# Kernel tuning notes

Measured on AMD Instinct MI355X. Metric: run time of the kernel, lower is better.

## Reference

```python
import jax, jax.numpy as jnp
import numpy as np

MEM_SIZE = 2048
CELL = 64
R_HEADS = 4
IN_SIZE = 512
IFACE = CELL * R_HEADS + CELL + 2 * CELL + 2 * R_HEADS + 5  # 461
DELTA = 1e-6
EPS = 1e-6


def setup_inputs() -> dict:
    key = jax.random.key(0)
    ks = jax.random.split(key, 8)
    b = 256
    return {
        'xi': jax.random.normal(ks[0], (b, IN_SIZE), jnp.float32),
        'W': jax.random.normal(ks[1], (IFACE, IN_SIZE), jnp.float32) * 0.05,
        'gamma': jnp.ones((IFACE,), jnp.float32),
        'beta': jnp.zeros((IFACE,), jnp.float32),
        'memory': jax.random.normal(ks[2], (b, MEM_SIZE, CELL), jnp.float32),
        'read_weights': jax.random.uniform(ks[3], (b, R_HEADS, MEM_SIZE), jnp.float32),
        'write_weights': jax.random.uniform(ks[4], (b, 1, MEM_SIZE), jnp.float32),
        'usage': jax.random.uniform(ks[5], (b, MEM_SIZE), jnp.float32),
    }


def _cosine(mem, keys):
    # mem: (b,m,c), keys: (b,k,c) -> (b,k,m)
    mem_n = mem / (jnp.linalg.norm(mem, axis=-1, keepdims=True) + EPS)
    key_n = keys / (jnp.linalg.norm(keys, axis=-1, keepdims=True) + EPS)
    return jnp.einsum('bkc,bmc->bkm', key_n, mem_n)


def reference(xi, W, gamma, beta, memory, read_weights, write_weights, usage):
    b = xi.shape[0]
    r, k, w, m = R_HEADS, CELL, CELL, MEM_SIZE

    # interface projection + GroupNorm(1, C) over channel dim
    itf = xi @ W.T
    mu = jnp.mean(itf, axis=1, keepdims=True)
    var = jnp.var(itf, axis=1, keepdims=True)
    itf = (itf - mu) / jnp.sqrt(var + 1e-5) * gamma + beta

    c = 0
    read_keys = jnp.tanh(itf[:, c:c + r * k].reshape(b, r, k)); c += r * k
    read_strengths = jax.nn.softplus(itf[:, c:c + r]); c += r
    write_key = jnp.tanh(itf[:, c:c + k].reshape(b, 1, k)); c += k
    write_strength = jax.nn.softplus(itf[:, c]).reshape(b, 1); c += 1
    erase_vec = jax.nn.sigmoid(itf[:, c:c + w].reshape(b, 1, w)); c += w
    write_vec = jnp.tanh(itf[:, c:c + w].reshape(b, 1, w)); c += w
    free_gates = jax.nn.sigmoid(itf[:, c:c + r]); c += r
    alloc_gate = jax.nn.softmax(itf[:, c:c + 3], axis=1); c += 3
    write_gate = jax.nn.sigmoid(itf[:, c]).reshape(b, 1)

    # ---- usage update ----
    u = usage + (1 - usage) * (1 - jnp.prod(1 - write_weights, axis=1))
    psi = jnp.prod(1 - free_gates[:, :, None] * read_weights, axis=1)  # (b,m)
    u = u * psi

    # ---- content weighting for write ----
    wcw = jax.nn.softmax(_cosine(memory, write_key) * write_strength[:, :, None], axis=2)  # (b,1,m)

    # ---- allocation ----
    u2 = DELTA + (1 - DELTA) * u
    idx = jnp.argsort(u2, axis=1)                              # ascending usage (phi)
    su = jnp.take_along_axis(u2, idx, axis=1)                  # sorted usage
    cp = jnp.cumprod(jnp.concatenate([jnp.ones((b, 1), u2.dtype), su], axis=1), axis=1)[:, :-1]
    sa = (1 - su) * cp
    inv = jnp.argsort(idx, axis=1)                             # inverse permutation (phi_rev)
    alloc = jnp.take_along_axis(sa, inv, axis=1)               # (b,m)

    # ---- write weighting ----
    fw = (alloc_gate[:, 0:1] * jnp.mean(read_weights, axis=1)
          + alloc_gate[:, 1:2] * alloc
          + alloc_gate[:, 2:3] * wcw[:, 0])
    ww = (write_gate * fw)[:, None, :]                         # (b,1,m)

    # ---- memory write (erase + add) ----
    reset_gate = jnp.prod(1 - ww[:, :, :, None] * erase_vec[:, :, None, :], axis=1)  # (b,m,w)
    mem = memory * reset_gate + jnp.einsum('bm,bw->bmw', ww[:, 0], write_vec[:, 0])

    # ---- read ----
    rw = jax.nn.softmax(_cosine(mem, read_keys) * read_strengths[:, :, None], axis=2)  # (b,r,m)
    read_vectors = jnp.einsum('brm,bmw->brw', rw, mem)         # (b,r,w)
    return read_vectors
```

## Files before the change

### kernel.cpp

```cpp
#include <hip/hip_runtime.h>
#include <math.h>

#define MM    2048
#define CC    64
#define RH    4
#define NIF   461
#define INS   512
#define EPSN  1e-6f

typedef unsigned long long u64;

#define OFF_P     ((size_t)0)
#define OFF_U2    ((size_t)131072)
#define OFF_MRW   ((size_t)655360)
#define OFF_ALLOC ((size_t)1179648)
#define OFF_SCAL  ((size_t)1703936)

__global__ __launch_bounds__(512) void k1_interface(
    const float* __restrict__ xi, const float* __restrict__ W,
    const float* __restrict__ gamma, const float* __restrict__ beta,
    const float* __restrict__ read_w, const float* __restrict__ write_w,
    const float* __restrict__ usage, float* __restrict__ ws)
{
  const int b = blockIdx.x, tid = threadIdx.x;
  const int lane = tid & 63, wid = tid >> 6;
  __shared__ __align__(16) float s_xi[512], s_itf[512], s_act[512];
  __shared__ float sRed[24];

  s_xi[tid] = xi[(size_t)b*INS + tid];
  __syncthreads();

  {
    const float4 x0 = ((const float4*)s_xi)[lane*2];
    const float4 x1 = ((const float4*)s_xi)[lane*2+1];
    for (int col = wid; col < NIF; col += 8) {
      const float4* Wr = (const float4*)(W + (size_t)col*INS);
      float4 a0 = Wr[lane*2], a1 = Wr[lane*2+1];
      float p = a0.x*x0.x + a0.y*x0.y + a0.z*x0.z + a0.w*x0.w
              + a1.x*x1.x + a1.y*x1.y + a1.z*x1.z + a1.w*x1.w;
      #pragma unroll
      for (int off=1; off<64; off<<=1) p += __shfl_xor(p, off);
      if (lane==0) s_itf[col] = p;
    }
  }
  __syncthreads();

  {
    float v = (tid < NIF) ? s_itf[tid] : 0.f;
    float s = v, q = v*v;
    #pragma unroll
    for (int off=1; off<64; off<<=1) { s += __shfl_xor(s,off); q += __shfl_xor(q,off); }
    if (lane==0){ sRed[wid] = s; sRed[8+wid] = q; }
    __syncthreads();
    if (tid==0){
      float ts=0.f, tq=0.f;
      for (int i=0;i<8;i++){ ts+=sRed[i]; tq+=sRed[8+i]; }
      float mean = ts/(float)NIF;
      float var  = tq/(float)NIF - mean*mean;
      sRed[16]=mean; sRed[17]=rsqrtf(var+1e-5f);
    }
    __syncthreads();
    float mean = sRed[16], rstd = sRed[17];
    if (tid < NIF) {
      float g = (s_itf[tid]-mean)*rstd*gamma[tid] + beta[tid];
      float a;
      if      (tid < 256) a = tanhf(g);
      else if (tid < 260) a = fmaxf(g,0.f) + log1pf(expf(-fabsf(g)));
      else if (tid < 324) a = tanhf(g);
      else if (tid ==324) a = fmaxf(g,0.f) + log1pf(expf(-fabsf(g)));
      else if (tid < 389) a = 1.f/(1.f+expf(-g));
      else if (tid < 453) a = tanhf(g);
      else if (tid < 457) a = 1.f/(1.f+expf(-g));
      else if (tid < 460) a = g;
      else                a = 1.f/(1.f+expf(-g));
      s_act[tid] = a;
    }
  }
  __syncthreads();

  float* P = ws + OFF_P + (size_t)b*512;
  if (wid < 4) {
    float t = s_act[wid*64 + lane];
    float q = t*t;
    #pragma unroll
    for (int off=1; off<64; off<<=1) q += __shfl_xor(q,off);
    P[wid*64+lane] = t * (s_act[256+wid] / (sqrtf(q) + EPSN));
  } else if (wid == 4) {
    float t = s_act[260+lane];
    float q = t*t;
    #pragma unroll
    for (int off=1; off<64; off<<=1) q += __shfl_xor(q,off);
    P[256+lane] = t * (s_act[324] / (sqrtf(q) + EPSN));
  } else if (wid == 5) {
    P[320+lane] = s_act[325+lane];
    P[384+lane] = s_act[389+lane];
  } else if (wid == 6 && lane == 0) {
    float a0=s_act[457], a1=s_act[458], a2=s_act[459];
    float mx = fmaxf(a0, fmaxf(a1,a2));
    float e0=expf(a0-mx), e1=expf(a1-mx), e2=expf(a2-mx);
    float is = 1.f/(e0+e1+e2);
    P[448]=e0*is; P[449]=e1*is; P[450]=e2*is; P[451]=s_act[460];
  }

  {
    const float4* us4 = (const float4*)(usage   + (size_t)b*MM);
    const float4* wr4 = (const float4*)(write_w + (size_t)b*MM);
    const float4* rw4 = (const float4*)(read_w  + (size_t)b*RH*MM);
    const float fg0=s_act[453], fg1=s_act[454], fg2=s_act[455], fg3=s_act[456];
    float4 u = us4[tid], w = wr4[tid];
    float4 r0 = rw4[tid], r1 = rw4[512+tid], r2 = rw4[1024+tid], r3 = rw4[1536+tid];
    float4 mr, u2o;
    mr.x = 0.25f*(r0.x+r1.x+r2.x+r3.x);
    mr.y = 0.25f*(r0.y+r1.y+r2.y+r3.y);
    mr.z = 0.25f*(r0.z+r1.z+r2.z+r3.z);
    mr.w = 0.25f*(r0.w+r1.w+r2.w+r3.w);
    #define U2C(comp)                                                           \
    { float uu  = u.comp + (1.f-u.comp)*w.comp;                                 \
      float psi = (1.f-fg0*r0.comp)*(1.f-fg1*r1.comp)*(1.f-fg2*r2.comp)*(1.f-fg3*r3.comp); \
      u2o.comp = 1e-6f + (1.f-1e-6f)*(uu*psi); }
    U2C(x) U2C(y) U2C(z) U2C(w)
    #undef U2C
    ((float4*)(ws + OFF_MRW + (size_t)b*MM))[tid] = mr;
    ((float4*)(ws + OFF_U2  + (size_t)b*MM))[tid] = u2o;
  }
}

__global__ __launch_bounds__(256) void k2_fused(
    const float* __restrict__ memory, float* __restrict__ ws)
{
  __shared__ __align__(16) u64 sKeys[2048];
  __shared__ float sT[260];
  const int tid = threadIdx.x;

  if (blockIdx.x < 256) {
    const int b = blockIdx.x;
    const int lane = tid & 63, w = tid >> 6;
    const float* u2p = ws + OFF_U2 + (size_t)b*MM;
    for (int i = tid; i < MM; i += 256)
      sKeys[i] = ((u64)__float_as_uint(u2p[i])<<32) | (unsigned)i;
    __syncthreads();

    for (int k = 2; k <= MM; k <<= 1) {
      for (int j = k >> 1; j > 0; j >>= 1) {
        #pragma unroll 4
        for (int c = tid; c < MM/2; c += 256) {
          int i   = ((c & ~(j-1)) << 1) | (c & (j-1));
          int ixj = i | j;
          u64 a = sKeys[i], d = sKeys[ixj];
          bool up = ((i & k) == 0);
          if ((a > d) == up) { sKeys[i] = d; sKeys[ixj] = a; }
        }
        __syncthreads();
      }
    }

    float p[8];
    {
      float run = 1.f;
      #pragma unroll
      for (int e = 0; e < 8; ++e) {
        float su = __uint_as_float((unsigned)(sKeys[tid*8+e]>>32));
        run *= su; p[e] = run;
      }
      sT[tid] = run;
    }
    __syncthreads();
    float v = sT[tid];
    float incl = v;
    #pragma unroll
    for (int off=1; off<64; off<<=1) {
      float n = __shfl_up(incl, off);
      if (lane >= off) incl *= n;
    }
    float excl = __shfl_up(incl, 1);
    if (lane == 0) excl = 1.f;
    if (lane == 63) sT[256 + w] = incl;
    __syncthreads();
    float base = 1.f;
    for (int ww2 = 0; ww2 < w; ++ww2) base *= sT[256 + ww2];
    float E = base * excl;

    float* allocp = ws + OFF_ALLOC + (size_t)b*MM;
    #pragma unroll
    for (int e = 0; e < 8; ++e) {
      u64 kk = sKeys[tid*8+e];
      float su = __uint_as_float((unsigned)(kk>>32));
      unsigned idx = (unsigned)(kk & 0xFFFFFFFFu);
      float cp = E * (e ? p[e-1] : 1.f);
      allocp[idx] = (1.f - su) * cp;
    }
  } else {
    const int f = blockIdx.x - 256;
    const int b = f >> 3, slice = f & 7;
    const int q = tid & 7, rowg = tid >> 3;
    const float* P = ws + OFF_P + (size_t)b*512;
    const float4 wkA = ((const float4*)(P+256))[q*2], wkB = ((const float4*)(P+256))[q*2+1];
    const float4 eA  = ((const float4*)(P+320))[q*2], eB  = ((const float4*)(P+320))[q*2+1];
    const float4 wvA = ((const float4*)(P+384))[q*2], wvB = ((const float4*)(P+384))[q*2+1];
    const float4 k0A = ((const float4*)P)[      q*2], k0B = ((const float4*)P)[      q*2+1];
    const float4 k1A = ((const float4*)P)[ 16 + q*2], k1B = ((const float4*)P)[ 16 + q*2+1];
    const float4 k2A = ((const float4*)P)[ 32 + q*2], k2B = ((const float4*)P)[ 32 + q*2+1];
    const float4 k3A = ((const float4*)P)[ 48 + q*2], k3B = ((const float4*)P)[ 48 + q*2+1];
    const float4* mem4 = (const float4*)(memory + (size_t)b*MM*CC) + (size_t)slice*256*16;
    float4* sc4 = (float4*)(ws + OFF_SCAL) + ((size_t)b*MM + slice*256)*4;

    for (int it = 0; it < 8; ++it) {
      int m = it*32 + rowg;
      float4 vA = mem4[m*16 + q*2], vB = mem4[m*16 + q*2+1];
      float4 veA, veB;
      veA.x=vA.x*eA.x; veA.y=vA.y*eA.y; veA.z=vA.z*eA.z; veA.w=vA.w*eA.w;
      veB.x=vB.x*eB.x; veB.y=vB.y*eB.y; veB.z=vB.z*eB.z; veB.w=vB.w*eB.w;
      #define DOT(a,b) (a.x*b.x + a.y*b.y + a.z*b.z + a.w*b.w)
      float S  = DOT(vA,wkA) + DOT(vB,wkB);
      float A  = DOT(vA,vA)  + DOT(vB,vB);
      float B  = DOT(veA,vA) + DOT(veB,vB);
      float C  = DOT(veA,veA)+ DOT(veB,veB);
      float D  = DOT(vA,wvA) + DOT(vB,wvB);
      float E  = DOT(veA,wvA)+ DOT(veB,wvB);
      float G0 = DOT(vA,k0A) + DOT(vB,k0B);
      float G1 = DOT(vA,k1A) + DOT(vB,k1B);
      float G2 = DOT(vA,k2A) + DOT(vB,k2B);
      float G3 = DOT(vA,k3A) + DOT(vB,k3B);
      float H0 = DOT(veA,k0A)+ DOT(veB,k0B);
      float H1 = DOT(veA,k1A)+ DOT(veB,k1B);
      float H2 = DOT(veA,k2A)+ DOT(veB,k2B);
      float H3 = DOT(veA,k3A)+ DOT(veB,k3B);
      #undef DOT
      #pragma unroll
      for (int off=1; off<8; off<<=1) {
        S += __shfl_xor(S,off);   A += __shfl_xor(A,off);
        B += __shfl_xor(B,off);   C += __shfl_xor(C,off);
        D += __shfl_xor(D,off);   E += __shfl_xor(E,off);
        G0 += __shfl_xor(G0,off); G1 += __shfl_xor(G1,off);
        G2 += __shfl_xor(G2,off); G3 += __shfl_xor(G3,off);
        H0 += __shfl_xor(H0,off); H1 += __shfl_xor(H1,off);
        H2 += __shfl_xor(H2,off); H3 += __shfl_xor(H3,off);
      }
      if (q == 0) {
        float4 o0; o0.x=S;  o0.y=A;  o0.z=B;  o0.w=C;
        float4 o1; o1.x=D;  o1.y=E;  o1.z=0;  o1.w=0;
        float4 o2; o2.x=G0; o2.y=G1; o2.z=G2; o2.w=G3;
        float4 o3; o3.x=H0; o3.y=H1; o3.z=H2; o3.w=H3;
        sc4[m*4+0]=o0; sc4[m*4+1]=o1; sc4[m*4+2]=o2; sc4[m*4+3]=o3;
      }
    }
  }
}

__global__ __launch_bounds__(256) void k3_fused(
    const float* __restrict__ memory, float* __restrict__ ws,
    float* __restrict__ out)
{
  const int slice = blockIdx.x >> 8, b = blockIdx.x & 255;
  const int tid = threadIdx.x, lane = tid & 63, w = tid >> 6;
  __shared__ __align__(16) float bufA[2048];
  __shared__ float bufB[256*5];
  __shared__ __align__(16) float ldsP[4*16*32];
  __shared__ float sR[48];
  __shared__ float sKF[8];

  const float* P = ws + OFF_P + (size_t)b*512;
  const float4* sc4 = (const float4*)(ws + OFF_SCAL + (size_t)b*MM*16);

  if (tid < 64) {
    float wv = P[384+tid];
    float p0=wv*P[tid], p1=wv*P[64+tid], p2=wv*P[128+tid], p3=wv*P[192+tid], f=wv*wv;
    #pragma unroll
    for (int off=1; off<64; off<<=1) {
      p0+=__shfl_xor(p0,off); p1+=__shfl_xor(p1,off); p2+=__shfl_xor(p2,off);
      p3+=__shfl_xor(p3,off); f+=__shfl_xor(f,off);
    }
    if (tid==0){ sKF[0]=p0; sKF[1]=p1; sKF[2]=p2; sKF[3]=p3; sKF[4]=f; }
  }

  float ls = 0.f;
  #pragma unroll
  for (int k = 0; k < 8; ++k) {
    int m = tid + k*256;
    float4 s0 = sc4[m*4];
    float ew = expf(s0.x / (sqrtf(s0.y)+EPSN));
    bufA[m] = ew;
    ls += ew;
  }
  #pragma unroll
  for (int off=1; off<64; off<<=1) ls += __shfl_xor(ls,off);
  if (lane==0) sR[w] = ls;
  __syncthreads();
  const float invW = 1.f/(sR[0]+sR[1]+sR[2]+sR[3]);

  const float ag0=P[448], ag1=P[449], ag2=P[450], wg=P[451];
  const float K0=sKF[0], K1=sKF[1], K2=sKF[2], K3=sKF[3], F=sKF[4];
  const float* mrwp = ws + OFF_MRW   + (size_t)b*MM;
  const float* alp  = ws + OFF_ALLOC + (size_t)b*MM;

  float h0=0.f,h1=0.f,h2=0.f,h3=0.f, g0=0.f,g1=0.f,g2=0.f,g3=0.f;
  #pragma unroll
  for (int k = 0; k < 8; ++k) {
    int m = tid + k*256;
    float wwv = wg*(ag0*mrwp[m] + ag1*alp[m] + ag2*bufA[m]*invW);
    float4 s0 = sc4[m*4], s1 = sc4[m*4+1], sG = sc4[m*4+2], sH = sc4[m*4+3];
    float nsq = s0.y + 2.f*wwv*(s1.x - s0.z) + wwv*wwv*(s0.w - 2.f*s1.y + F);
    float rstd = 1.f/(sqrtf(fmaxf(nsq,0.f))+EPSN);
    float e0 = expf((sG.x + wwv*(K0 - sH.x))*rstd);
    float e1 = expf((sG.y + wwv*(K1 - sH.y))*rstd);
    float e2 = expf((sG.z + wwv*(K2 - sH.z))*rstd);
    float e3 = expf((sG.w + wwv*(K3 - sH.w))*rstd);
    h0+=e0; h1+=e1; h2+=e2; h3+=e3;
    g0+=e0*wwv; g1+=e1*wwv; g2+=e2*wwv; g3+=e3*wwv;
    if (k == slice) {
      bufB[tid]=e0; bufB[256+tid]=e1; bufB[512+tid]=e2; bufB[768+tid]=e3;
      bufB[1024+tid]=wwv;
    }
  }
  #pragma unroll
  for (int off=1; off<64; off<<=1) {
    h0+=__shfl_xor(h0,off); h1+=__shfl_xor(h1,off);
    h2+=__shfl_xor(h2,off); h3+=__shfl_xor(h3,off);
    g0+=__shfl_xor(g0,off); g1+=__shfl_xor(g1,off);
    g2+=__shfl_xor(g2,off); g3+=__shfl_xor(g3,off);
  }
  if (lane==0){
    sR[8 +w*8+0]=h0; sR[8 +w*8+1]=h1; sR[8 +w*8+2]=h2; sR[8 +w*8+3]=h3;
    sR[8 +w*8+4]=g0; sR[8 +w*8+5]=g1; sR[8 +w*8+6]=g2; sR[8 +w*8+7]=g3;
  }
  __syncthreads();
  const float i0 = 1.f/(sR[8] +sR[16]+sR[24]+sR[32]);
  const float i1 = 1.f/(sR[9] +sR[17]+sR[25]+sR[33]);
  const float i2 = 1.f/(sR[10]+sR[18]+sR[26]+sR[34]);
  const float i3 = 1.f/(sR[11]+sR[19]+sR[27]+sR[35]);
  const float cr0 = (sR[12]+sR[20]+sR[28]+sR[36])*i0;
  const float cr1 = (sR[13]+sR[21]+sR[29]+sR[37])*i1;
  const float cr2 = (sR[14]+sR[22]+sR[30]+sR[38])*i2;
  const float cr3 = (sR[15]+sR[23]+sR[31]+sR[39])*i3;

  {
    float e0=bufB[tid], e1=bufB[256+tid], e2=bufB[512+tid], e3=bufB[768+tid];
    float wwv=bufB[1024+tid];
    float a0=e0*i0, a1=e1*i1, a2=e2*i2, a3=e3*i3;
    bufA[tid*8+0]=a0; bufA[tid*8+1]=a1; bufA[tid*8+2]=a2; bufA[tid*8+3]=a3;
    bufA[tid*8+4]=a0*wwv; bufA[tid*8+5]=a1*wwv; bufA[tid*8+6]=a2*wwv; bufA[tid*8+7]=a3*wwv;
  }
  __syncthreads();

  const int rq = lane >> 4, cq = lane & 15;
  const float4* mem4 = (const float4*)(memory + (size_t)b*MM*CC) + (size_t)slice*256*16;
  float4 acc[8];
  #pragma unroll
  for (int j=0;j<8;++j){ acc[j].x=0;acc[j].y=0;acc[j].z=0;acc[j].w=0; }
  #pragma unroll 4
  for (int i = 0; i < 16; ++i) {
    int m = w*64 + i*4 + rq;
    float4 v = mem4[m*16 + cq];
    float4 wa = *(const float4*)&bufA[m*8];
    float4 wb = *(const float4*)&bufA[m*8+4];
    #define ACC(j, s) { acc[j].x += (s)*v.x; acc[j].y += (s)*v.y; acc[j].z += (s)*v.z; acc[j].w += (s)*v.w; }
    ACC(0, wa.x) ACC(1, wa.y) ACC(2, wa.z) ACC(3, wa.w)
    ACC(4, wb.x) ACC(5, wb.y) ACC(6, wb.z) ACC(7, wb.w)
    #undef ACC
  }
  #pragma unroll
  for (int j=0;j<8;++j){
    #pragma unroll
    for (int off=16; off<64; off<<=1) {
      acc[j].x += __shfl_xor(acc[j].x, off);
      acc[j].y += __shfl_xor(acc[j].y, off);
      acc[j].z += __shfl_xor(acc[j].z, off);
      acc[j].w += __shfl_xor(acc[j].w, off);
    }
  }
  if (rq == 0) {
    float4* p4 = (float4*)&ldsP[(w*16 + cq)*32];
    #pragma unroll
    for (int j=0;j<8;++j) p4[j] = acc[j];
  }
  __syncthreads();

  {
    int jj = tid >> 6;
    int c  = tid & 63;
    int cq2 = c >> 2, ci = c & 3;
    float s1 = 0.f, s2 = 0.f;
    #pragma unroll
    for (int g=0; g<4; ++g) {
      s1 += ldsP[(g*16 + cq2)*32 +  jj*4    + ci];
      s2 += ldsP[(g*16 + cq2)*32 + (jj+4)*4 + ci];
    }
    float crv = (jj==0)?cr0:((jj==1)?cr1:((jj==2)?cr2:cr3));
    float val = s1 - P[320+c]*s2 + crv*P[384+c]*0.125f;
    atomicAdd(&out[((size_t)b<<8) + jj*64 + c], val);
  }
}

extern "C" void kernel_launch(void* const* d_in, const int* in_sizes, int n_in,
                              void* d_out, int out_size, void* d_ws, size_t ws_size,
                              hipStream_t stream) {
  const float* xi      = (const float*)d_in[0];
  const float* W       = (const float*)d_in[1];
  const float* gamma   = (const float*)d_in[2];
  const float* beta    = (const float*)d_in[3];
  const float* memory  = (const float*)d_in[4];
  const float* read_w  = (const float*)d_in[5];
  const float* write_w = (const float*)d_in[6];
  const float* usage   = (const float*)d_in[7];
  float* ws  = (float*)d_ws;
  float* out = (float*)d_out;

  hipMemsetAsync(out, 0, (size_t)out_size*sizeof(float), stream);
  k1_interface<<<dim3(256), dim3(512), 0, stream>>>(xi, W, gamma, beta, read_w, write_w, usage, ws);
  k2_fused   <<<dim3(2304), dim3(256), 0, stream>>>(memory, ws);
  k3_fused   <<<dim3(2048), dim3(256), 0, stream>>>(memory, ws, out);
}
```

Before: 155.9 us.

## Fuse all stages into one cooperative persistent kernel with grid syncs

```diff
diff --git a/kernel.cpp b/kernel.cpp
--- a/kernel.cpp
+++ b/kernel.cpp
@@ -1,9 +1,11 @@
 #include <hip/hip_runtime.h>
+#include <hip/hip_cooperative_groups.h>
 #include <math.h>
+
+namespace cg = cooperative_groups;
 
 #define MM    2048
 #define CC    64
-#define RH    4
 #define NIF   461
 #define INS   512
 #define EPSN  1e-6f
@@ -11,162 +13,176 @@
 typedef unsigned long long u64;
 
 #define OFF_P     ((size_t)0)
-#define OFF_U2    ((size_t)131072)
-#define OFF_MRW   ((size_t)655360)
-#define OFF_ALLOC ((size_t)1179648)
-#define OFF_SCAL  ((size_t)1703936)
-
-__global__ __launch_bounds__(512) void k1_interface(
+#define OFF_ITF   ((size_t)131072)
+#define OFF_ALLOC ((size_t)249856)
+#define OFF_MRW   ((size_t)774144)
+#define OFF_SUMS  ((size_t)1298432)
+#define OFF_SCAL  ((size_t)1302528)
+#define OFF_W8    ((size_t)9691136)
+
+__device__ __forceinline__ float actfn(int c, float g){
+  if (c < 256)  return tanhf(g);
+  if (c < 260)  return fmaxf(g,0.f) + log1pf(expf(-fabsf(g)));
+  if (c < 324)  return tanhf(g);
+  if (c == 324) return fmaxf(g,0.f) + log1pf(expf(-fabsf(g)));
+  if (c < 389)  return 1.f/(1.f+expf(-g));
+  if (c < 453)  return tanhf(g);
+  if (c < 457)  return 1.f/(1.f+expf(-g));
+  if (c < 460)  return g;
+  return 1.f/(1.f+expf(-g));
+}
+
+__global__ __launch_bounds__(256,2) void dnc_all(
     const float* __restrict__ xi, const float* __restrict__ W,
     const float* __restrict__ gamma, const float* __restrict__ beta,
-    const float* __restrict__ read_w, const float* __restrict__ write_w,
-    const float* __restrict__ usage, float* __restrict__ ws)
+    const float* __restrict__ memory, const float* __restrict__ read_w,
+    const float* __restrict__ write_w, const float* __restrict__ usage,
+    float* __restrict__ ws, float* __restrict__ out)
 {
-  const int b = blockIdx.x, tid = threadIdx.x;
-  const int lane = tid & 63, wid = tid >> 6;
-  __shared__ __align__(16) float s_xi[512], s_itf[512], s_act[512];
-  __shared__ float sRed[24];
-
-  s_xi[tid] = xi[(size_t)b*INS + tid];
+  cg::grid_group grid = cg::this_grid();
+  const int bid = blockIdx.x, tid = threadIdx.x;
+  const int lane = tid & 63, wvid = tid >> 6;
+  const int b = bid & 255, half = bid >> 8;
+
+  __shared__ __align__(16) unsigned char sMem[19456];
+  __shared__ float sR[64];
+  u64*   keysL = (u64*)sMem;
+  float* sTL   = (float*)(sMem + 16384);
+  float* sactL = (float*)(sMem + 17424);
+  float* sxiL  = (float*)sMem;
+  float* sW8   = (float*)sMem;
+  float* ldsP  = (float*)(sMem + 8192);
+
+  if (tid < 128) out[((size_t)bid<<7) + tid] = 0.f;
+  if (bid < 256 && tid < 16) ws[OFF_SUMS + (size_t)bid*16 + tid] = 0.f;
+  sxiL[tid]     = xi[(size_t)b*INS + tid];
+  sxiL[tid+256] = xi[(size_t)b*INS + tid + 256];
   __syncthreads();
-
   {
-    const float4 x0 = ((const float4*)s_xi)[lane*2];
-    const float4 x1 = ((const float4*)s_xi)[lane*2+1];
-    for (int col = wid; col < NIF; col += 8) {
+    const float4 x0 = ((const float4*)sxiL)[lane*2];
+    const float4 x1 = ((const float4*)sxiL)[lane*2+1];
+    const int cbase = half*232;
+    const int cend  = (cbase+232 < NIF) ? cbase+232 : NIF;
+    for (int col = cbase + wvid; col < cend; col += 4) {
       const float4* Wr = (const float4*)(W + (size_t)col*INS);
       float4 a0 = Wr[lane*2], a1 = Wr[lane*2+1];
       float p = a0.x*x0.x + a0.y*x0.y + a0.z*x0.z + a0.w*x0.w
               + a1.x*x1.x + a1.y*x1.y + a1.z*x1.z + a1.w*x1.w;
       #pragma unroll
       for (int off=1; off<64; off<<=1) p += __shfl_xor(p, off);
-      if (lane==0) s_itf[col] = p;
+      if (lane==0) ws[OFF_ITF + (size_t)b*464 + col] = p;
     }
   }
-  __syncthreads();
-
-  {
-    float v = (tid < NIF) ? s_itf[tid] : 0.f;
-    float s = v, q = v*v;
+  __threadfence();
+  grid.sync();
+
+  if (bid < 256) {
+    const float* itf = ws + OFF_ITF + (size_t)b*464;
+    float v1 = (tid < NIF) ? itf[tid] : 0.f;
+    float v2 = (tid+256 < NIF) ? itf[tid+256] : 0.f;
+    float s = v1+v2, q = v1*v1+v2*v2;
     #pragma unroll
-    for (int off=1; off<64; off<<=1) { s += __shfl_xor(s,off); q += __shfl_xor(q,off); }
-    if (lane==0){ sRed[wid] = s; sRed[8+wid] = q; }
+    for (int off=1; off<64; off<<=1){ s += __shfl_xor(s,off); q += __shfl_xor(q,off); }
+    if (lane==0){ sR[wvid]=s; sR[8+wvid]=q; }
     __syncthreads();
     if (tid==0){
-      float ts=0.f, tq=0.f;
-      for (int i=0;i<8;i++){ ts+=sRed[i]; tq+=sRed[8+i]; }
+      float ts=sR[0]+sR[1]+sR[2]+sR[3], tq=sR[8]+sR[9]+sR[10]+sR[11];
       float mean = ts/(float)NIF;
       float var  = tq/(float)NIF - mean*mean;
-      sRed[16]=mean; sRed[17]=rsqrtf(var+1e-5f);
-    }
-    __syncthreads();
-    float mean = sRed[16], rstd = sRed[17];
-    if (tid < NIF) {
-      float g = (s_itf[tid]-mean)*rstd*gamma[tid] + beta[tid];
-      float a;
-      if      (tid < 256) a = tanhf(g);
-      else if (tid < 260) a = fmaxf(g,0.f) + log1pf(expf(-fabsf(g)));
-      else if (tid < 324) a = tanhf(g);
-      else if (tid ==324) a = fmaxf(g,0.f) + log1pf(expf(-fabsf(g)));
-      else if (tid < 389) a = 1.f/(1.f+expf(-g));
-      else if (tid < 453) a = tanhf(g);
-      else if (tid < 457) a = 1.f/(1.f+expf(-g));
-      else if (tid < 460) a = g;
-      else                a = 1.f/(1.f+expf(-g));
-      s_act[tid] = a;
-    }
-  }
-  __syncthreads();
-
-  float* P = ws + OFF_P + (size_t)b*512;
-  if (wid < 4) {
-    float t = s_act[wid*64 + lane];
-    float q = t*t;
-    #pragma unroll
-    for (int off=1; off<64; off<<=1) q += __shfl_xor(q,off);
-    P[wid*64+lane] = t * (s_act[256+wid] / (sqrtf(q) + EPSN));
-  } else if (wid == 4) {
-    float t = s_act[260+lane];
-    float q = t*t;
-    #pragma unroll
-    for (int off=1; off<64; off<<=1) q += __shfl_xor(q,off);
-    P[256+lane] = t * (s_act[324] / (sqrtf(q) + EPSN));
-  } else if (wid == 5) {
-    P[320+lane] = s_act[325+lane];
-    P[384+lane] = s_act[389+lane];
-  } else if (wid == 6 && lane == 0) {
-    float a0=s_act[457], a1=s_act[458], a2=s_act[459];
-    float mx = fmaxf(a0, fmaxf(a1,a2));
-    float e0=expf(a0-mx), e1=expf(a1-mx), e2=expf(a2-mx);
-    float is = 1.f/(e0+e1+e2);
-    P[448]=e0*is; P[449]=e1*is; P[450]=e2*is; P[451]=s_act[460];
-  }
-
-  {
-    const float4* us4 = (const float4*)(usage   + (size_t)b*MM);
-    const float4* wr4 = (const float4*)(write_w + (size_t)b*MM);
-    const float4* rw4 = (const float4*)(read_w  + (size_t)b*RH*MM);
-    const float fg0=s_act[453], fg1=s_act[454], fg2=s_act[455], fg3=s_act[456];
-    float4 u = us4[tid], w = wr4[tid];
-    float4 r0 = rw4[tid], r1 = rw4[512+tid], r2 = rw4[1024+tid], r3 = rw4[1536+tid];
-    float4 mr, u2o;
-    mr.x = 0.25f*(r0.x+r1.x+r2.x+r3.x);
-    mr.y = 0.25f*(r0.y+r1.y+r2.y+r3.y);
-    mr.z = 0.25f*(r0.z+r1.z+r2.z+r3.z);
-    mr.w = 0.25f*(r0.w+r1.w+r2.w+r3.w);
-    #define U2C(comp)                                                           \
-    { float uu  = u.comp + (1.f-u.comp)*w.comp;                                 \
-      float psi = (1.f-fg0*r0.comp)*(1.f-fg1*r1.comp)*(1.f-fg2*r2.comp)*(1.f-fg3*r3.comp); \
-      u2o.comp = 1e-6f + (1.f-1e-6f)*(uu*psi); }
-    U2C(x) U2C(y) U2C(z) U2C(w)
-    #undef U2C
-    ((float4*)(ws + OFF_MRW + (size_t)b*MM))[tid] = mr;
-    ((float4*)(ws + OFF_U2  + (size_t)b*MM))[tid] = u2o;
-  }
-}
-
-__global__ __launch_bounds__(256) void k2_fused(
-    const float* __restrict__ memory, float* __restrict__ ws)
-{
-  __shared__ __align__(16) u64 sKeys[2048];
-  __shared__ float sT[260];
-  const int tid = threadIdx.x;
-
-  if (blockIdx.x < 256) {
-    const int b = blockIdx.x;
-    const int lane = tid & 63, w = tid >> 6;
-    const float* u2p = ws + OFF_U2 + (size_t)b*MM;
-    for (int i = tid; i < MM; i += 256)
-      sKeys[i] = ((u64)__float_as_uint(u2p[i])<<32) | (unsigned)i;
-    __syncthreads();
-
-    for (int k = 2; k <= MM; k <<= 1) {
-      for (int j = k >> 1; j > 0; j >>= 1) {
+      sR[16]=mean; sR[17]=rsqrtf(var+1e-5f);
+    }
+    __syncthreads();
+    float mean=sR[16], rstd=sR[17];
+    if (tid < NIF)     sactL[tid]     = actfn(tid,     (v1-mean)*rstd*gamma[tid]    +beta[tid]);
+    if (tid+256 < NIF) sactL[tid+256] = actfn(tid+256, (v2-mean)*rstd*gamma[tid+256]+beta[tid+256]);
+    __syncthreads();
+
+    float* P = ws + OFF_P + (size_t)b*512;
+    {
+      float t0 = sactL[wvid*64 + lane];
+      float qq = t0*t0;
+      #pragma unroll
+      for (int off=1; off<64; off<<=1) qq += __shfl_xor(qq,off);
+      float fk = t0 * (sactL[256+wvid]/(sqrtf(qq)+EPSN));
+      P[wvid*64+lane] = fk;
+      float kk = fk * sactL[389+lane];
+      #pragma unroll
+      for (int off=1; off<64; off<<=1) kk += __shfl_xor(kk,off);
+      if (lane==0) P[452+wvid] = kk;
+    }
+    if (wvid==0) {
+      float t0 = sactL[260+lane];
+      float qq = t0*t0;
+      #pragma unroll
+      for (int off=1; off<64; off<<=1) qq += __shfl_xor(qq,off);
+      P[256+lane] = t0 * (sactL[324]/(sqrtf(qq)+EPSN));
+      float wvv = sactL[389+lane];
+      float ff = wvv*wvv;
+      #pragma unroll
+      for (int off=1; off<64; off<<=1) ff += __shfl_xor(ff,off);
+      if (lane==0) P[456]=ff;
+    } else if (wvid==1) {
+      P[320+lane] = sactL[325+lane];
+    } else if (wvid==2) {
+      P[384+lane] = sactL[389+lane];
+    } else if (wvid==3 && lane==0) {
+      float a0=sactL[457], a1=sactL[458], a2=sactL[459];
+      float mx = fmaxf(a0, fmaxf(a1,a2));
+      float e0=expf(a0-mx), e1=expf(a1-mx), e2=expf(a2-mx);
+      float is = 1.f/(e0+e1+e2);
+      P[448]=e0*is; P[449]=e1*is; P[450]=e2*is; P[451]=sactL[460];
+    }
+    {
+      const float4* us4 = (const float4*)(usage   + (size_t)b*MM);
+      const float4* wr4 = (const float4*)(write_w + (size_t)b*MM);
+      const float4* rw4 = (const float4*)(read_w  + (size_t)b*4*MM);
+      const float fg0=sactL[453], fg1=sactL[454], fg2=sactL[455], fg3=sactL[456];
+      #pragma unroll
+      for (int k=0;k<2;k++){
+        int i4 = tid + k*256;
+        float4 u = us4[i4], w2 = wr4[i4];
+        float4 r0 = rw4[i4], r1 = rw4[512+i4], r2 = rw4[1024+i4], r3 = rw4[1536+i4];
+        float4 mr;
+        mr.x = 0.25f*(r0.x+r1.x+r2.x+r3.x);
+        mr.y = 0.25f*(r0.y+r1.y+r2.y+r3.y);
+        mr.z = 0.25f*(r0.z+r1.z+r2.z+r3.z);
+        mr.w = 0.25f*(r0.w+r1.w+r2.w+r3.w);
+        ((float4*)(ws + OFF_MRW + (size_t)b*MM))[i4] = mr;
+        #define U2C(comp, off)                                                   \
+        { float uu  = u.comp + (1.f-u.comp)*w2.comp;                             \
+          float psi = (1.f-fg0*r0.comp)*(1.f-fg1*r1.comp)*(1.f-fg2*r2.comp)*(1.f-fg3*r3.comp); \
+          float u2v = 1e-6f + (1.f-1e-6f)*(uu*psi);                              \
+          keysL[i4*4+off] = ((u64)__float_as_uint(u2v)<<32) | (unsigned)(i4*4+off); }
+        U2C(x,0) U2C(y,1) U2C(z,2) U2C(w,3)
+        #undef U2C
+      }
+    }
+    __syncthreads();
+    for (int k2 = 2; k2 <= MM; k2 <<= 1) {
+      for (int j = k2 >> 1; j > 0; j >>= 1) {
         #pragma unroll 4
         for (int c = tid; c < MM/2; c += 256) {
           int i   = ((c & ~(j-1)) << 1) | (c & (j-1));
           int ixj = i | j;
-          u64 a = sKeys[i], d = sKeys[ixj];
-          bool up = ((i & k) == 0);
-          if ((a > d) == up) { sKeys[i] = d; sKeys[ixj] = a; }
+          u64 a = keysL[i], d = keysL[ixj];
+          bool up = ((i & k2) == 0);
+          if ((a > d) == up) { keysL[i] = d; keysL[ixj] = a; }
         }
         __syncthreads();
       }
     }
-
-    float p[8];
+    float p8[8];
     {
       float run = 1.f;
       #pragma unroll
-      for (int e = 0; e < 8; ++e) {
-        float su = __uint_as_float((unsigned)(sKeys[tid*8+e]>>32));
-        run *= su; p[e] = run;
-      }
-      sT[tid] = run;
-    }
-    __syncthreads();
-    float v = sT[tid];
-    float incl = v;
+      for (int e=0;e<8;++e){
+        float su = __uint_as_float((unsigned)(keysL[tid*8+e]>>32));
+        run *= su; p8[e] = run;
+      }
+      sTL[tid] = run;
+    }
+    __syncthreads();
+    float vv = sTL[tid], incl = vv;
     #pragma unroll
     for (int off=1; off<64; off<<=1) {
       float n = __shfl_up(incl, off);
@@ -174,26 +190,27 @@
     }
     float excl = __shfl_up(incl, 1);
     if (lane == 0) excl = 1.f;
-    if (lane == 63) sT[256 + w] = incl;
+    if (lane == 63) sTL[256 + wvid] = incl;
     __syncthreads();
     float base = 1.f;
-    for (int ww2 = 0; ww2 < w; ++ww2) base *= sT[256 + ww2];
-    float E = base * excl;
-
+    for (int w2i = 0; w2i < wvid; ++w2i) base *= sTL[256 + w2i];
+    float Ex = base * excl;
     float* allocp = ws + OFF_ALLOC + (size_t)b*MM;
     #pragma unroll
-    for (int e = 0; e < 8; ++e) {
-      u64 kk = sKeys[tid*8+e];
+    for (int e=0;e<8;++e){
+      u64 kk = keysL[tid*8+e];
       float su = __uint_as_float((unsigned)(kk>>32));
       unsigned idx = (unsigned)(kk & 0xFFFFFFFFu);
-      float cp = E * (e ? p[e-1] : 1.f);
+      float cp = Ex * (e ? p8[e-1] : 1.f);
       allocp[idx] = (1.f - su) * cp;
     }
-  } else {
-    const int f = blockIdx.x - 256;
-    const int b = f >> 3, slice = f & 7;
+  }
+  __threadfence();
+  grid.sync();
+
+  {
+    const float* P = ws + OFF_P + (size_t)b*512;
     const int q = tid & 7, rowg = tid >> 3;
-    const float* P = ws + OFF_P + (size_t)b*512;
     const float4 wkA = ((const float4*)(P+256))[q*2], wkB = ((const float4*)(P+256))[q*2+1];
     const float4 eA  = ((const float4*)(P+320))[q*2], eB  = ((const float4*)(P+320))[q*2+1];
     const float4 wvA = ((const float4*)(P+384))[q*2], wvB = ((const float4*)(P+384))[q*2+1];
@@ -201,193 +218,177 @@
     const float4 k1A = ((const float4*)P)[ 16 + q*2], k1B = ((const float4*)P)[ 16 + q*2+1];
     const float4 k2A = ((const float4*)P)[ 32 + q*2], k2B = ((const float4*)P)[ 32 + q*2+1];
     const float4 k3A = ((const float4*)P)[ 48 + q*2], k3B = ((const float4*)P)[ 48 + q*2+1];
-    const float4* mem4 = (const float4*)(memory + (size_t)b*MM*CC) + (size_t)slice*256*16;
-    float4* sc4 = (float4*)(ws + OFF_SCAL) + ((size_t)b*MM + slice*256)*4;
-
-    for (int it = 0; it < 8; ++it) {
-      int m = it*32 + rowg;
-      float4 vA = mem4[m*16 + q*2], vB = mem4[m*16 + q*2+1];
-      float4 veA, veB;
-      veA.x=vA.x*eA.x; veA.y=vA.y*eA.y; veA.z=vA.z*eA.z; veA.w=vA.w*eA.w;
-      veB.x=vB.x*eB.x; veB.y=vB.y*eB.y; veB.z=vB.z*eB.z; veB.w=vB.w*eB.w;
-      #define DOT(a,b) (a.x*b.x + a.y*b.y + a.z*b.z + a.w*b.w)
-      float S  = DOT(vA,wkA) + DOT(vB,wkB);
-      float A  = DOT(vA,vA)  + DOT(vB,vB);
-      float B  = DOT(veA,vA) + DOT(veB,vB);
-      float C  = DOT(veA,veA)+ DOT(veB,veB);
-      float D  = DOT(vA,wvA) + DOT(vB,wvB);
-      float E  = DOT(veA,wvA)+ DOT(veB,wvB);
-      float G0 = DOT(vA,k0A) + DOT(vB,k0B);
-      float G1 = DOT(vA,k1A) + DOT(vB,k1B);
-      float G2 = DOT(vA,k2A) + DOT(vB,k2B);
-      float G3 = DOT(vA,k3A) + DOT(vB,k3B);
-      float H0 = DOT(veA,k0A)+ DOT(veB,k0B);
-      float H1 = DOT(veA,k1A)+ DOT(veB,k1B);
-      float H2 = DOT(veA,k2A)+ DOT(veB,k2B);
-      float H3 = DOT(veA,k3A)+ DOT(veB,k3B);
-      #undef DOT
-      #pragma unroll
-      for (int off=1; off<8; off<<=1) {
-        S += __shfl_xor(S,off);   A += __shfl_xor(A,off);
-        B += __shfl_xor(B,off);   C += __shfl_xor(C,off);
-        D += __shfl_xor(D,off);   E += __shfl_xor(E,off);
-        G0 += __shfl_xor(G0,off); G1 += __shfl_xor(G1,off);
-        G2 += __shfl_xor(G2,off); G3 += __shfl_xor(G3,off);
-        H0 += __shfl_xor(H0,off); H1 += __shfl_xor(H1,off);
-        H2 += __shfl_xor(H2,off); H3 += __shfl_xor(H3,off);
-      }
-      if (q == 0) {
-        float4 o0; o0.x=S;  o0.y=A;  o0.z=B;  o0.w=C;
-        float4 o1; o1.x=D;  o1.y=E;  o1.z=0;  o1.w=0;
-        float4 o2; o2.x=G0; o2.y=G1; o2.z=G2; o2.w=G3;
-        float4 o3; o3.x=H0; o3.y=H1; o3.z=H2; o3.w=H3;
-        sc4[m*4+0]=o0; sc4[m*4+1]=o1; sc4[m*4+2]=o2; sc4[m*4+3]=o3;
-      }
-    }
+    const float4* mem4 = (const float4*)(memory + (size_t)b*MM*CC);
+    float4* scal4 = (float4*)(ws + OFF_SCAL) + (size_t)b*2048*4;
+    float ewsum = 0.f;
+    for (int si=0; si<4; ++si) {
+      const int s = half*4 + si;
+      for (int it=0; it<8; ++it) {
+        int m = it*32 + rowg;
+        int mg = s*256 + m;
+        float4 vA = mem4[mg*16 + q*2], vB = mem4[mg*16 + q*2+1];
+        float4 veA, veB;
+        veA.x=vA.x*eA.x; veA.y=vA.y*eA.y; veA.z=vA.z*eA.z; veA.w=vA.w*eA.w;
+        veB.x=vB.x*eB.x; veB.y=vB.y*eB.y; veB.z=vB.z*eB.z; veB.w=vB.w*eB.w;
+        #define DOT(a,c) (a.x*c.x + a.y*c.y + a.z*c.z + a.w*c.w)
+        float S  = DOT(vA,wkA) + DOT(vB,wkB);
+        float A  = DOT(vA,vA)  + DOT(vB,vB);
+        float B  = DOT(veA,vA) + DOT(veB,vB);
+        float C  = DOT(veA,veA)+ DOT(veB,veB);
+        float D  = DOT(vA,wvA) + DOT(vB,wvB);
+        float E  = DOT(veA,wvA)+ DOT(veB,wvB);
+        float G0 = DOT(vA,k0A) + DOT(vB,k0B);
+        float G1 = DOT(vA,k1A) + DOT(vB,k1B);
+        float G2 = DOT(vA,k2A) + DOT(vB,k2B);
+        float G3 = DOT(vA,k3A) + DOT(vB,k3B);
+        float H0 = DOT(veA,k0A)+ DOT(veB,k0B);
+        float H1 = DOT(veA,k1A)+ DOT(veB,k1B);
+        float H2 = DOT(veA,k2A)+ DOT(veB,k2B);
+        float H3 = DOT(veA,k3A)+ DOT(veB,k3B);
+        #undef DOT
+        #pragma unroll
+        for (int off=1; off<8; off<<=1) {
+          S += __shfl_xor(S,off);   A += __shfl_xor(A,off);
+          B += __shfl_xor(B,off);   C += __shfl_xor(C,off);
+          D += __shfl_xor(D,off);   E += __shfl_xor(E,off);
+          G0 += __shfl_xor(G0,off); G1 += __shfl_xor(G1,off);
+          G2 += __shfl_xor(G2,off); G3 += __shfl_xor(G3,off);
+          H0 += __shfl_xor(H0,off); H1 += __shfl_xor(H1,off);
+          H2 += __shfl_xor(H2,off); H3 += __shfl_xor(H3,off);
+        }
+        if (q == 0) {
+          float ew = expf(S / (sqrtf(A)+EPSN));
+          ewsum += ew;
+          float4 o0; o0.x=S;  o0.y=A;  o0.z=B;  o0.w=C;
+          float4 o1; o1.x=D;  o1.y=E;  o1.z=ew; o1.w=0.f;
+          float4 o2; o2.x=G0; o2.y=G1; o2.z=G2; o2.w=G3;
+          float4 o3; o3.x=H0; o3.y=H1; o3.z=H2; o3.w=H3;
+          scal4[mg*4+0]=o0; scal4[mg*4+1]=o1; scal4[mg*4+2]=o2; scal4[mg*4+3]=o3;
+        }
+      }
+    }
+    #pragma unroll
+    for (int off=1; off<64; off<<=1) ewsum += __shfl_xor(ewsum,off);
+    __syncthreads();
+    if (lane==0) sR[wvid] = ewsum;
+    __syncthreads();
+    if (tid==0) atomicAdd(&ws[OFF_SUMS + (size_t)b*16], sR[0]+sR[1]+sR[2]+sR[3]);
   }
-}
-
-__global__ __launch_bounds__(256) void k3_fused(
-    const float* __restrict__ memory, float* __restrict__ ws,
-    float* __restrict__ out)
-{
-  const int slice = blockIdx.x >> 8, b = blockIdx.x & 255;
-  const int tid = threadIdx.x, lane = tid & 63, w = tid >> 6;
-  __shared__ __align__(16) float bufA[2048];
-  __shared__ float bufB[256*5];
-  __shared__ __align__(16) float ldsP[4*16*32];
-  __shared__ float sR[48];
-  __shared__ float sKF[8];
-
-  const float* P = ws + OFF_P + (size_t)b*512;
-  const float4* sc4 = (const float4*)(ws + OFF_SCAL + (size_t)b*MM*16);
-
-  if (tid < 64) {
-    float wv = P[384+tid];
-    float p0=wv*P[tid], p1=wv*P[64+tid], p2=wv*P[128+tid], p3=wv*P[192+tid], f=wv*wv;
+  __threadfence();
+  grid.sync();
+
+  {
+    const float* P = ws + OFF_P + (size_t)b*512;
+    const float ag0=P[448], ag1=P[449], ag2=P[450], wg=P[451];
+    const float K0=P[452], K1=P[453], K2v=P[454], K3v=P[455], F=P[456];
+    const float invW = 1.f / ws[OFF_SUMS + (size_t)b*16];
+    float h[4]={0,0,0,0}, g[4]={0,0,0,0};
+    for (int si=0; si<4; ++si) {
+      const int r = (half*4+si)*256 + tid;
+      const float4* row = (const float4*)(ws + OFF_SCAL) + ((size_t)b*2048 + r)*4;
+      float4 s0=row[0], s1=row[1], sG=row[2], sH=row[3];
+      float al = ws[OFF_ALLOC + (size_t)b*MM + r];
+      float mr = ws[OFF_MRW   + (size_t)b*MM + r];
+      float wwv = wg*(ag0*mr + ag1*al + ag2*s1.z*invW);
+      float nsq = s0.y + 2.f*wwv*(s1.x - s0.z) + wwv*wwv*(s0.w - 2.f*s1.y + F);
+      float rstd = 1.f/(sqrtf(fmaxf(nsq,0.f))+EPSN);
+      float e0 = expf((sG.x + wwv*(K0 -sH.x))*rstd);
+      float e1 = expf((sG.y + wwv*(K1 -sH.y))*rstd);
+      float e2 = expf((sG.z + wwv*(K2v-sH.z))*rstd);
+      float e3 = expf((sG.w + wwv*(K3v-sH.w))*rstd);
+      float4 oa; oa.x=e0; oa.y=e1; oa.z=e2; oa.w=e3;
+      float4 og; og.x=e0*wwv; og.y=e1*wwv; og.z=e2*wwv; og.w=e3*wwv;
+      float4* w84 = (float4*)(ws + OFF_W8) + ((size_t)b*2048 + r)*2;
+      w84[0]=oa; w84[1]=og;
+      h[0]+=e0; h[1]+=e1; h[2]+=e2; h[3]+=e3;
+      g[0]+=og.x; g[1]+=og.y; g[2]+=og.z; g[3]+=og.w;
+    }
     #pragma unroll
     for (int off=1; off<64; off<<=1) {
-      p0+=__shfl_xor(p0,off); p1+=__shfl_xor(p1,off); p2+=__shfl_xor(p2,off);
-      p3+=__shfl_xor(p3,off); f+=__shfl_xor(f,off);
-    }
-    if (tid==0){ sKF[0]=p0; sKF[1]=p1; sKF[2]=p2; sKF[3]=p3; sKF[4]=f; }
+      #pragma unroll
+      for (int r2=0;r2<4;++r2){ h[r2]+=__shfl_xor(h[r2],off); g[r2]+=__shfl_xor(g[r2],off); }
+    }
+    __syncthreads();
+    if (lane==0){
+      #pragma unroll
+      for (int r2=0;r2<4;++r2){ sR[wvid*8+r2]=h[r2]; sR[wvid*8+4+r2]=g[r2]; }
+    }
+    __syncthreads();
+    if (tid < 8){
+      float ssum = sR[tid] + sR[8+tid] + sR[16+tid] + sR[24+tid];
+      atomicAdd(&ws[OFF_SUMS + (size_t)b*16 + 1 + tid], ssum);
+    }
   }
-
-  float ls = 0.f;
-  #pragma unroll
-  for (int k = 0; k < 8; ++k) {
-    int m = tid + k*256;
-    float4 s0 = sc4[m*4];
-    float ew = expf(s0.x / (sqrtf(s0.y)+EPSN));
-    bufA[m] = ew;
-    ls += ew;
-  }
-  #pragma unroll
-  for (int off=1; off<64; off<<=1) ls += __shfl_xor(ls,off);
-  if (lane==0) sR[w] = ls;
-  __syncthreads();
-  const float invW = 1.f/(sR[0]+sR[1]+sR[2]+sR[3]);
-
-  const float ag0=P[448], ag1=P[449], ag2=P[450], wg=P[451];
-  const float K0=sKF[0], K1=sKF[1], K2=sKF[2], K3=sKF[3], F=sKF[4];
-  const float* mrwp = ws + OFF_MRW   + (size_t)b*MM;
-  const float* alp  = ws + OFF_ALLOC + (size_t)b*MM;
-
-  float h0=0.f,h1=0.f,h2=0.f,h3=0.f, g0=0.f,g1=0.f,g2=0.f,g3=0.f;
-  #pragma unroll
-  for (int k = 0; k < 8; ++k) {
-    int m = tid + k*256;
-    float wwv = wg*(ag0*mrwp[m] + ag1*alp[m] + ag2*bufA[m]*invW);
-    float4 s0 = sc4[m*4], s1 = sc4[m*4+1], sG = sc4[m*4+2], sH = sc4[m*4+3];
-    float nsq = s0.y + 2.f*wwv*(s1.x - s0.z) + wwv*wwv*(s0.w - 2.f*s1.y + F);
-    float rstd = 1.f/(sqrtf(fmaxf(nsq,0.f))+EPSN);
-    float e0 = expf((sG.x + wwv*(K0 - sH.x))*rstd);
-    float e1 = expf((sG.y + wwv*(K1 - sH.y))*rstd);
-    float e2 = expf((sG.z + wwv*(K2 - sH.z))*rstd);
-    float e3 = expf((sG.w + wwv*(K3 - sH.w))*rstd);
-    h0+=e0; h1+=e1; h2+=e2; h3+=e3;
-    g0+=e0*wwv; g1+=e1*wwv; g2+=e2*wwv; g3+=e3*wwv;
-    if (k == slice) {
-      bufB[tid]=e0; bufB[256+tid]=e1; bufB[512+tid]=e2; bufB[768+tid]=e3;
-      bufB[1024+tid]=wwv;
-    }
-  }
-  #pragma unroll
-  for (int off=1; off<64; off<<=1) {
-    h0+=__shfl_xor(h0,off); h1+=__shfl_xor(h1,off);
-    h2+=__shfl_xor(h2,off); h3+=__shfl_xor(h3,off);
-    g0+=__shfl_xor(g0,off); g1+=__shfl_xor(g1,off);
-    g2+=__shfl_xor(g2,off); g3+=__shfl_xor(g3,off);
-  }
-  if (lane==0){
-    sR[8 +w*8+0]=h0; sR[8 +w*8+1]=h1; sR[8 +w*8+2]=h2; sR[8 +w*8+3]=h3;
-    sR[8 +w*8+4]=g0; sR[8 +w*8+5]=g1; sR[8 +w*8+6]=g2; sR[8 +w*8+7]=g3;
-  }
-  __syncthreads();
-  const float i0 = 1.f/(sR[8] +sR[16]+sR[24]+sR[32]);
-  const float i1 = 1.f/(sR[9] +sR[17]+sR[25]+sR[33]);
-  const float i2 = 1.f/(sR[10]+sR[18]+sR[26]+sR[34]);
-  const float i3 = 1.f/(sR[11]+sR[19]+sR[27]+sR[35]);
-  const float cr0 = (sR[12]+sR[20]+sR[28]+sR[36])*i0;
-  const float cr1 = (sR[13]+sR[21]+sR[29]+sR[37])*i1;
-  const float cr2 = (sR[14]+sR[22]+sR[30]+sR[38])*i2;
-  const float cr3 = (sR[15]+sR[23]+sR[31]+sR[39])*i3;
+  __threadfence();
+  grid.sync();
 
   {
-    float e0=bufB[tid], e1=bufB[256+tid], e2=bufB[512+tid], e3=bufB[768+tid];
-    float wwv=bufB[1024+tid];
-    float a0=e0*i0, a1=e1*i1, a2=e2*i2, a3=e3*i3;
-    bufA[tid*8+0]=a0; bufA[tid*8+1]=a1; bufA[tid*8+2]=a2; bufA[tid*8+3]=a3;
-    bufA[tid*8+4]=a0*wwv; bufA[tid*8+5]=a1*wwv; bufA[tid*8+6]=a2*wwv; bufA[tid*8+7]=a3*wwv;
-  }
-  __syncthreads();
-
-  const int rq = lane >> 4, cq = lane & 15;
-  const float4* mem4 = (const float4*)(memory + (size_t)b*MM*CC) + (size_t)slice*256*16;
-  float4 acc[8];
-  #pragma unroll
-  for (int j=0;j<8;++j){ acc[j].x=0;acc[j].y=0;acc[j].z=0;acc[j].w=0; }
-  #pragma unroll 4
-  for (int i = 0; i < 16; ++i) {
-    int m = w*64 + i*4 + rq;
-    float4 v = mem4[m*16 + cq];
-    float4 wa = *(const float4*)&bufA[m*8];
-    float4 wb = *(const float4*)&bufA[m*8+4];
-    #define ACC(j, s) { acc[j].x += (s)*v.x; acc[j].y += (s)*v.y; acc[j].z += (s)*v.z; acc[j].w += (s)*v.w; }
-    ACC(0, wa.x) ACC(1, wa.y) ACC(2, wa.z) ACC(3, wa.w)
-    ACC(4, wb.x) ACC(5, wb.y) ACC(6, wb.z) ACC(7, wb.w)
-    #undef ACC
-  }
-  #pragma unroll
-  for (int j=0;j<8;++j){
-    #pragma unroll
-    for (int off=16; off<64; off<<=1) {
-      acc[j].x += __shfl_xor(acc[j].x, off);
-      acc[j].y += __shfl_xor(acc[j].y, off);
-      acc[j].z += __shfl_xor(acc[j].z, off);
-      acc[j].w += __shfl_xor(acc[j].w, off);
-    }
-  }
-  if (rq == 0) {
-    float4* p4 = (float4*)&ldsP[(w*16 + cq)*32];
-    #pragma unroll
-    for (int j=0;j<8;++j) p4[j] = acc[j];
-  }
-  __syncthreads();
-
-  {
-    int jj = tid >> 6;
-    int c  = tid & 63;
-    int cq2 = c >> 2, ci = c & 3;
-    float s1 = 0.f, s2 = 0.f;
-    #pragma unroll
-    for (int g=0; g<4; ++g) {
-      s1 += ldsP[(g*16 + cq2)*32 +  jj*4    + ci];
-      s2 += ldsP[(g*16 + cq2)*32 + (jj+4)*4 + ci];
-    }
-    float crv = (jj==0)?cr0:((jj==1)?cr1:((jj==2)?cr2:cr3));
-    float val = s1 - P[320+c]*s2 + crv*P[384+c]*0.125f;
-    atomicAdd(&out[((size_t)b<<8) + jj*64 + c], val);
+    const float* P = ws + OFF_P + (size_t)b*512;
+    const float i0 = 1.f/ws[OFF_SUMS+(size_t)b*16+1];
+    const float i1 = 1.f/ws[OFF_SUMS+(size_t)b*16+2];
+    const float i2 = 1.f/ws[OFF_SUMS+(size_t)b*16+3];
+    const float i3 = 1.f/ws[OFF_SUMS+(size_t)b*16+4];
+    const float cr0 = ws[OFF_SUMS+(size_t)b*16+5]*i0;
+    const float cr1 = ws[OFF_SUMS+(size_t)b*16+6]*i1;
+    const float cr2 = ws[OFF_SUMS+(size_t)b*16+7]*i2;
+    const float cr3 = ws[OFF_SUMS+(size_t)b*16+8]*i3;
+    const int rq = lane >> 4, cq = lane & 15;
+    const float4* mem4 = (const float4*)(memory + (size_t)b*MM*CC);
+    for (int si=0; si<4; ++si) {
+      const int s = half*4 + si;
+      {
+        const float4* g8 = (const float4*)(ws + OFF_W8) + ((size_t)b*2048 + s*256)*2;
+        ((float4*)sW8)[tid]     = g8[tid];
+        ((float4*)sW8)[tid+256] = g8[tid+256];
+      }
+      __syncthreads();
+      float4 acc[8];
+      #pragma unroll
+      for (int j=0;j<8;++j){ acc[j].x=0;acc[j].y=0;acc[j].z=0;acc[j].w=0; }
+      #pragma unroll 4
+      for (int i=0;i<16;++i){
+        int m = wvid*64 + i*4 + rq;
+        float4 v = mem4[(s*256+m)*16 + cq];
+        float4 wa = *(const float4*)&sW8[m*8];
+        float4 wb = *(const float4*)&sW8[m*8+4];
+        #define ACC(j, sc) { acc[j].x += (sc)*v.x; acc[j].y += (sc)*v.y; acc[j].z += (sc)*v.z; acc[j].w += (sc)*v.w; }
+        ACC(0, wa.x) ACC(1, wa.y) ACC(2, wa.z) ACC(3, wa.w)
+        ACC(4, wb.x) ACC(5, wb.y) ACC(6, wb.z) ACC(7, wb.w)
+        #undef ACC
+      }
+      #pragma unroll
+      for (int j=0;j<8;++j){
+        #pragma unroll
+        for (int off=16; off<64; off<<=1) {
+          acc[j].x += __shfl_xor(acc[j].x, off);
+          acc[j].y += __shfl_xor(acc[j].y, off);
+          acc[j].z += __shfl_xor(acc[j].z, off);
+          acc[j].w += __shfl_xor(acc[j].w, off);
+        }
+      }
+      if (rq == 0) {
+        float4* p4 = (float4*)&ldsP[(wvid*16 + cq)*32];
+        #pragma unroll
+        for (int j=0;j<8;++j) p4[j] = acc[j];
+      }
+      __syncthreads();
+      {
+        int jj = tid >> 6, c = tid & 63;
+        int cq2 = c >> 2, ci = c & 3;
+        float s1 = 0.f, s2 = 0.f;
+        #pragma unroll
+        for (int g4=0; g4<4; ++g4) {
+          s1 += ldsP[(g4*16 + cq2)*32 +  jj   *4 + ci];
+          s2 += ldsP[(g4*16 + cq2)*32 + (jj+4)*4 + ci];
+        }
+        float ir  = (jj==0)?i0:((jj==1)?i1:((jj==2)?i2:i3));
+        float crr = (jj==0)?cr0:((jj==1)?cr1:((jj==2)?cr2:cr3));
+        float val = ir*(s1 - P[320+c]*s2);
+        if (bid < 256 && si == 0) val += crr * P[384+c];
+        atomicAdd(&out[((size_t)b<<8) + tid], val);
+      }
+      __syncthreads();
+    }
   }
 }
 
@@ -405,8 +406,9 @@
   float* ws  = (float*)d_ws;
   float* out = (float*)d_out;
 
-  hipMemsetAsync(out, 0, (size_t)out_size*sizeof(float), stream);
-  k1_interface<<<dim3(256), dim3(512), 0, stream>>>(xi, W, gamma, beta, read_w, write_w, usage, ws);
-  k2_fused   <<<dim3(2304), dim3(256), 0, stream>>>(memory, ws);
-  k3_fused   <<<dim3(2048), dim3(256), 0, stream>>>(memory, ws, out);
+  void* args[] = { (void*)&xi, (void*)&W, (void*)&gamma, (void*)&beta,
+                   (void*)&memory, (void*)&read_w, (void*)&write_w, (void*)&usage,
+                   (void*)&ws, (void*)&out };
+  hipLaunchCooperativeKernel((const void*)dnc_all, dim3(512), dim3(256),
+                             args, 0, stream);
 }
```

New measurement: 590.2 us. +278.5%, slower.
